# Kernel tuning notes

Measured on AMD Instinct MI355X. Metric: run time of the kernel, lower is better.

## Reference

```python
import jax, jax.numpy as jnp
import numpy as np

NUM_SEGMENTS = 8192  # number of graphs in the batch (max(batch)+1 in the torch code)
EPS = 1e-10


def setup_inputs() -> dict:
    key = jax.random.key(0)
    k1, k2 = jax.random.split(key)
    N, D = 2_000_000, 32
    batch = jnp.sort(jax.random.randint(k1, (N,), 0, NUM_SEGMENTS, dtype=jnp.int64))
    x = jax.random.normal(k2, (N, D), dtype=jnp.float32)
    return {"batch": batch, "input": x}


def reference(batch, input):
    # segment-wise numerically-stable softmax over nodes sharing a batch id
    # seg_max: [S, D]; empty segments get -inf but are never gathered
    seg_max = jax.ops.segment_max(input, batch, num_segments=NUM_SEGMENTS)
    x = jnp.exp(input - seg_max[batch])            # [N, D]
    norm = jax.ops.segment_sum(x, batch, num_segments=NUM_SEGMENTS)[batch]  # [N, D]
    return x / (norm + EPS)
```

## Files before the change

### kernel.cpp

```cpp
#include <hip/hip_runtime.h>
#include <math.h>

#define NSEG 8192
#define D 32
#define EPSF 1e-10f
#define ROWS_CAP 512
#define BLK 256

__global__ void init_starts_kernel(int* __restrict__ seg_start, int N) {
    int s = blockIdx.x * blockDim.x + threadIdx.x;
    if (s <= NSEG) seg_start[s] = N;
}

__global__ void find_starts_kernel(const int* __restrict__ batch,
                                   int* __restrict__ seg_start, int N) {
    int i = blockIdx.x * blockDim.x + threadIdx.x;
    if (i >= N) return;
    int b = batch[i];
    int prev = (i == 0) ? -1 : batch[i - 1];
    for (int s = prev + 1; s <= b; ++s) seg_start[s] = i;
}

__device__ __forceinline__ float4 f4max(float4 a, float4 b) {
    return make_float4(fmaxf(a.x, b.x), fmaxf(a.y, b.y),
                       fmaxf(a.z, b.z), fmaxf(a.w, b.w));
}
__device__ __forceinline__ float4 f4add(float4 a, float4 b) {
    return make_float4(a.x + b.x, a.y + b.y, a.z + b.z, a.w + b.w);
}
__device__ __forceinline__ float4 shfl_xor_f4(float4 v, int mask) {
    return make_float4(__shfl_xor(v.x, mask, 64), __shfl_xor(v.y, mask, 64),
                       __shfl_xor(v.z, mask, 64), __shfl_xor(v.w, mask, 64));
}

__global__ __launch_bounds__(BLK, 2) void seg_softmax_kernel(
    const float* __restrict__ x, const int* __restrict__ seg_start,
    float* __restrict__ out)
{
    __shared__ float4 xbuf[ROWS_CAP * (D / 4)];
    __shared__ float4 red[4 * (D / 4)];

    const int s     = blockIdx.x;
    const int start = seg_start[s];
    const int end   = seg_start[s + 1];
    const int len   = end - start;
    if (len <= 0) return;

    const int tid  = (int)threadIdx.x;
    const int cg   = tid & 7;
    const int rg   = tid >> 3;
    const int wave = tid >> 6;
    const int lane = tid & 63;

    const float4* __restrict__ xin  = (const float4*)(x   + (size_t)start * D);
    float4* __restrict__       outv = (float4*)      (out + (size_t)start * D);

    const float4 neg_inf4 = make_float4(-INFINITY, -INFINITY, -INFINITY, -INFINITY);

    if (len <= ROWS_CAP) {
        float4 lmax = neg_inf4;
        for (int r = rg; r < len; r += 32) {
            float4 v = xin[r * 8 + cg];
            xbuf[r * 8 + cg] = v;
            lmax = f4max(lmax, v);
        }
        lmax = f4max(lmax, shfl_xor_f4(lmax, 8));
        lmax = f4max(lmax, shfl_xor_f4(lmax, 16));
        lmax = f4max(lmax, shfl_xor_f4(lmax, 32));
        if (lane < 8) red[wave * 8 + cg] = lmax;
        __syncthreads();
        float4 cmax = f4max(f4max(red[0 * 8 + cg], red[1 * 8 + cg]),
                            f4max(red[2 * 8 + cg], red[3 * 8 + cg]));
        __syncthreads();

        float4 lsum = make_float4(0.f, 0.f, 0.f, 0.f);
        for (int r = rg; r < len; r += 32) {
            float4 v = xbuf[r * 8 + cg];
            float4 e;
            e.x = __expf(v.x - cmax.x);
            e.y = __expf(v.y - cmax.y);
            e.z = __expf(v.z - cmax.z);
            e.w = __expf(v.w - cmax.w);
            xbuf[r * 8 + cg] = e;
            lsum = f4add(lsum, e);
        }
        lsum = f4add(lsum, shfl_xor_f4(lsum, 8));
        lsum = f4add(lsum, shfl_xor_f4(lsum, 16));
        lsum = f4add(lsum, shfl_xor_f4(lsum, 32));
        if (lane < 8) red[wave * 8 + cg] = lsum;
        __syncthreads();
        float4 csum = f4add(f4add(red[0 * 8 + cg], red[1 * 8 + cg]),
                            f4add(red[2 * 8 + cg], red[3 * 8 + cg]));
        float4 rnorm = make_float4(1.f / (csum.x + EPSF), 1.f / (csum.y + EPSF),
                                   1.f / (csum.z + EPSF), 1.f / (csum.w + EPSF));

        for (int r = rg; r < len; r += 32) {
            float4 e = xbuf[r * 8 + cg];
            e.x *= rnorm.x; e.y *= rnorm.y; e.z *= rnorm.z; e.w *= rnorm.w;
            outv[r * 8 + cg] = e;
        }
    } else {
        float4 lmax = neg_inf4;
        for (int r = rg; r < len; r += 32)
            lmax = f4max(lmax, xin[r * 8 + cg]);
        lmax = f4max(lmax, shfl_xor_f4(lmax, 8));
        lmax = f4max(lmax, shfl_xor_f4(lmax, 16));
        lmax = f4max(lmax, shfl_xor_f4(lmax, 32));
        if (lane < 8) red[wave * 8 + cg] = lmax;
        __syncthreads();
        float4 cmax = f4max(f4max(red[0 * 8 + cg], red[1 * 8 + cg]),
                            f4max(red[2 * 8 + cg], red[3 * 8 + cg]));
        __syncthreads();

        float4 lsum = make_float4(0.f, 0.f, 0.f, 0.f);
        for (int r = rg; r < len; r += 32) {
            float4 v = xin[r * 8 + cg];
            float4 e;
            e.x = __expf(v.x - cmax.x);
            e.y = __expf(v.y - cmax.y);
            e.z = __expf(v.z - cmax.z);
            e.w = __expf(v.w - cmax.w);
            outv[r * 8 + cg] = e;
            lsum = f4add(lsum, e);
        }
        lsum = f4add(lsum, shfl_xor_f4(lsum, 8));
        lsum = f4add(lsum, shfl_xor_f4(lsum, 16));
        lsum = f4add(lsum, shfl_xor_f4(lsum, 32));
        if (lane < 8) red[wave * 8 + cg] = lsum;
        __syncthreads();
        float4 csum = f4add(f4add(red[0 * 8 + cg], red[1 * 8 + cg]),
                            f4add(red[2 * 8 + cg], red[3 * 8 + cg]));
        float4 rnorm = make_float4(1.f / (csum.x + EPSF), 1.f / (csum.y + EPSF),
                                   1.f / (csum.z + EPSF), 1.f / (csum.w + EPSF));

        for (int r = rg; r < len; r += 32) {
            float4 e = outv[r * 8 + cg];
            e.x *= rnorm.x; e.y *= rnorm.y; e.z *= rnorm.z; e.w *= rnorm.w;
            outv[r * 8 + cg] = e;
        }
    }
}

extern "C" void kernel_launch(void* const* d_in, const int* in_sizes, int n_in,
                              void* d_out, int out_size, void* d_ws, size_t ws_size,
                              hipStream_t stream) {
    const int*   batch = (const int*)d_in[0];
    const float* x     = (const float*)d_in[1];
    float*       out   = (float*)d_out;
    const int    N     = in_sizes[0];

    int* seg_start = (int*)d_ws;

    init_starts_kernel<<<(NSEG + 1 + 255) / 256, 256, 0, stream>>>(seg_start, N);
    find_starts_kernel<<<(N + 255) / 256, 256, 0, stream>>>(batch, seg_start, N);
    seg_softmax_kernel<<<NSEG, BLK, 0, stream>>>(x, seg_start, out);
}
```

Measured before the change: 466.7 us.

## Assign one wave per segment with online softmax and drop LDS staging

Each wave now processes a whole segment, computing running max and rescaled sum in one pass (online softmax) and then re-reading input to write normalized output. The large shared-memory row buffer and block-level syncs are removed, and launch bounds rise to allow more resident blocks. This trades an extra global read of the input and extra exp work for higher occupancy and no barriers.

```diff
diff --git a/kernel.cpp b/kernel.cpp
--- a/kernel.cpp
+++ b/kernel.cpp
@@ -4,8 +4,8 @@
 #define NSEG 8192
 #define D 32
 #define EPSF 1e-10f
-#define ROWS_CAP 512
 #define BLK 256
+#define SEG_PER_BLK 4
 
 __global__ void init_starts_kernel(int* __restrict__ seg_start, int N) {
     int s = blockIdx.x * blockDim.x + threadIdx.x;
@@ -25,119 +25,65 @@
     return make_float4(fmaxf(a.x, b.x), fmaxf(a.y, b.y),
                        fmaxf(a.z, b.z), fmaxf(a.w, b.w));
 }
-__device__ __forceinline__ float4 f4add(float4 a, float4 b) {
-    return make_float4(a.x + b.x, a.y + b.y, a.z + b.z, a.w + b.w);
-}
 __device__ __forceinline__ float4 shfl_xor_f4(float4 v, int mask) {
     return make_float4(__shfl_xor(v.x, mask, 64), __shfl_xor(v.y, mask, 64),
                        __shfl_xor(v.z, mask, 64), __shfl_xor(v.w, mask, 64));
 }
 
-__global__ __launch_bounds__(BLK, 2) void seg_softmax_kernel(
+__global__ __launch_bounds__(BLK, 8) void seg_softmax_kernel(
     const float* __restrict__ x, const int* __restrict__ seg_start,
     float* __restrict__ out)
 {
-    __shared__ float4 xbuf[ROWS_CAP * (D / 4)];
-    __shared__ float4 red[4 * (D / 4)];
+    const int wave = (int)threadIdx.x >> 6;
+    const int lane = (int)threadIdx.x & 63;
+    const int s    = blockIdx.x * SEG_PER_BLK + wave;
 
-    const int s     = blockIdx.x;
     const int start = seg_start[s];
-    const int end   = seg_start[s + 1];
-    const int len   = end - start;
+    const int len   = seg_start[s + 1] - start;
     if (len <= 0) return;
 
-    const int tid  = (int)threadIdx.x;
-    const int cg   = tid & 7;
-    const int rg   = tid >> 3;
-    const int wave = tid >> 6;
-    const int lane = tid & 63;
+    const int cg = lane & 7;
+    const int rg = lane >> 3;
 
     const float4* __restrict__ xin  = (const float4*)(x   + (size_t)start * D);
     float4* __restrict__       outv = (float4*)      (out + (size_t)start * D);
 
-    const float4 neg_inf4 = make_float4(-INFINITY, -INFINITY, -INFINITY, -INFINITY);
+    float4 m = make_float4(-3.402823466e38f, -3.402823466e38f,
+                           -3.402823466e38f, -3.402823466e38f);
+    float4 l = make_float4(0.f, 0.f, 0.f, 0.f);
+    for (int r = rg; r < len; r += 8) {
+        float4 v = xin[r * 8 + cg];
+        float4 mn = f4max(m, v);
+        l.x = l.x * __expf(m.x - mn.x) + __expf(v.x - mn.x);
+        l.y = l.y * __expf(m.y - mn.y) + __expf(v.y - mn.y);
+        l.z = l.z * __expf(m.z - mn.z) + __expf(v.z - mn.z);
+        l.w = l.w * __expf(m.w - mn.w) + __expf(v.w - mn.w);
+        m = mn;
+    }
 
-    if (len <= ROWS_CAP) {
-        float4 lmax = neg_inf4;
-        for (int r = rg; r < len; r += 32) {
-            float4 v = xin[r * 8 + cg];
-            xbuf[r * 8 + cg] = v;
-            lmax = f4max(lmax, v);
-        }
-        lmax = f4max(lmax, shfl_xor_f4(lmax, 8));
-        lmax = f4max(lmax, shfl_xor_f4(lmax, 16));
-        lmax = f4max(lmax, shfl_xor_f4(lmax, 32));
-        if (lane < 8) red[wave * 8 + cg] = lmax;
-        __syncthreads();
-        float4 cmax = f4max(f4max(red[0 * 8 + cg], red[1 * 8 + cg]),
-                            f4max(red[2 * 8 + cg], red[3 * 8 + cg]));
-        __syncthreads();
+    #pragma unroll
+    for (int mask = 8; mask <= 32; mask <<= 1) {
+        float4 mo = shfl_xor_f4(m, mask);
+        float4 lo = shfl_xor_f4(l, mask);
+        float4 mn = f4max(m, mo);
+        l.x = l.x * __expf(m.x - mn.x) + lo.x * __expf(mo.x - mn.x);
+        l.y = l.y * __expf(m.y - mn.y) + lo.y * __expf(mo.y - mn.y);
+        l.z = l.z * __expf(m.z - mn.z) + lo.z * __expf(mo.z - mn.z);
+        l.w = l.w * __expf(m.w - mn.w) + lo.w * __expf(mo.w - mn.w);
+        m = mn;
+    }
 
-        float4 lsum = make_float4(0.f, 0.f, 0.f, 0.f);
-        for (int r = rg; r < len; r += 32) {
-            float4 v = xbuf[r * 8 + cg];
-            float4 e;
-            e.x = __expf(v.x - cmax.x);
-            e.y = __expf(v.y - cmax.y);
-            e.z = __expf(v.z - cmax.z);
-            e.w = __expf(v.w - cmax.w);
-            xbuf[r * 8 + cg] = e;
-            lsum = f4add(lsum, e);
-        }
-        lsum = f4add(lsum, shfl_xor_f4(lsum, 8));
-        lsum = f4add(lsum, shfl_xor_f4(lsum, 16));
-        lsum = f4add(lsum, shfl_xor_f4(lsum, 32));
-        if (lane < 8) red[wave * 8 + cg] = lsum;
-        __syncthreads();
-        float4 csum = f4add(f4add(red[0 * 8 + cg], red[1 * 8 + cg]),
-                            f4add(red[2 * 8 + cg], red[3 * 8 + cg]));
-        float4 rnorm = make_float4(1.f / (csum.x + EPSF), 1.f / (csum.y + EPSF),
-                                   1.f / (csum.z + EPSF), 1.f / (csum.w + EPSF));
+    const float4 rn = make_float4(1.f / (l.x + EPSF), 1.f / (l.y + EPSF),
+                                  1.f / (l.z + EPSF), 1.f / (l.w + EPSF));
 
-        for (int r = rg; r < len; r += 32) {
-            float4 e = xbuf[r * 8 + cg];
-            e.x *= rnorm.x; e.y *= rnorm.y; e.z *= rnorm.z; e.w *= rnorm.w;
-            outv[r * 8 + cg] = e;
-        }
-    } else {
-        float4 lmax = neg_inf4;
-        for (int r = rg; r < len; r += 32)
-            lmax = f4max(lmax, xin[r * 8 + cg]);
-        lmax = f4max(lmax, shfl_xor_f4(lmax, 8));
-        lmax = f4max(lmax, shfl_xor_f4(lmax, 16));
-        lmax = f4max(lmax, shfl_xor_f4(lmax, 32));
-        if (lane < 8) red[wave * 8 + cg] = lmax;
-        __syncthreads();
-        float4 cmax = f4max(f4max(red[0 * 8 + cg], red[1 * 8 + cg]),
-                            f4max(red[2 * 8 + cg], red[3 * 8 + cg]));
-        __syncthreads();
-
-        float4 lsum = make_float4(0.f, 0.f, 0.f, 0.f);
-        for (int r = rg; r < len; r += 32) {
-            float4 v = xin[r * 8 + cg];
-            float4 e;
-            e.x = __expf(v.x - cmax.x);
-            e.y = __expf(v.y - cmax.y);
-            e.z = __expf(v.z - cmax.z);
-            e.w = __expf(v.w - cmax.w);
-            outv[r * 8 + cg] = e;
-            lsum = f4add(lsum, e);
-        }
-        lsum = f4add(lsum, shfl_xor_f4(lsum, 8));
-        lsum = f4add(lsum, shfl_xor_f4(lsum, 16));
-        lsum = f4add(lsum, shfl_xor_f4(lsum, 32));
-        if (lane < 8) red[wave * 8 + cg] = lsum;
-        __syncthreads();
-        float4 csum = f4add(f4add(red[0 * 8 + cg], red[1 * 8 + cg]),
-                            f4add(red[2 * 8 + cg], red[3 * 8 + cg]));
-        float4 rnorm = make_float4(1.f / (csum.x + EPSF), 1.f / (csum.y + EPSF),
-                                   1.f / (csum.z + EPSF), 1.f / (csum.w + EPSF));
-
-        for (int r = rg; r < len; r += 32) {
-            float4 e = outv[r * 8 + cg];
-            e.x *= rnorm.x; e.y *= rnorm.y; e.z *= rnorm.z; e.w *= rnorm.w;
-            outv[r * 8 + cg] = e;
-        }
+    for (int r = rg; r < len; r += 8) {
+        float4 v = xin[r * 8 + cg];
+        float4 e;
+        e.x = __expf(v.x - m.x) * rn.x;
+        e.y = __expf(v.y - m.y) * rn.y;
+        e.z = __expf(v.z - m.z) * rn.z;
+        e.w = __expf(v.w - m.w) * rn.w;
+        outv[r * 8 + cg] = e;
     }
 }
 
@@ -153,5 +99,5 @@
 
     init_starts_kernel<<<(NSEG + 1 + 255) / 256, 256, 0, stream>>>(seg_start, N);
     find_starts_kernel<<<(N + 255) / 256, 256, 0, stream>>>(batch, seg_start, N);
-    seg_softmax_kernel<<<NSEG, BLK, 0, stream>>>(x, seg_start, out);
+    seg_softmax_kernel<<<NSEG / SEG_PER_BLK, BLK, 0, stream>>>(x, seg_start, out);
 }
```

Result: slower. 484.4 us (+3.8%).
